# Kernel tuning notes

Hardware: AMD Instinct MI355X
Metric: run time of the kernel (lower is better)

## Reference

```python
import jax, jax.numpy as jnp
import numpy as np

EPS = 1e-8

def _center(G):
    # Double-centering: H @ G @ H with H = I - 11^T/n, expressed as mean subtraction.
    # Identical math to the torch H-matmul version, O(n^2) instead of O(n^3).
    row = jnp.mean(G, axis=-1, keepdims=True)
    col = jnp.mean(G, axis=-2, keepdims=True)
    tot = jnp.mean(G, axis=(-2, -1), keepdims=True)
    return G - row - col + tot


def setup_inputs() -> dict:
    key = jax.random.key(0)
    k1, k2 = jax.random.split(key)
    B, L, H, M = 32, 128, 512, 512
    x = jax.random.normal(k1, (B, L, H), dtype=jnp.float32)
    # nn.Embedding.from_pretrained(torch.normal(-0.01, 0.2, (M, L*H)))
    centroid_w = jax.random.normal(k2, (M, L * H), dtype=jnp.float32) * 0.2 - 0.01
    return {"x": x, "centroid_w": centroid_w}


def reference(x, centroid_w):
    B, L, H = x.shape
    M = centroid_w.shape[0]
    cent = centroid_w.reshape(M, L, H)

    # Centered linear Grams
    Cx = _center(jnp.einsum('blh,bkh->blk', x, x))        # (B, L, L)
    Cy = _center(jnp.einsum('mlh,mkh->mlk', cent, cent))  # (M, L, L)

    # linear HSIC: sum over LxL of elementwise product -> (B, M)
    hsic = jnp.einsum('bij,mij->bm', Cx, Cy)
    vx = jnp.sqrt(jnp.sum(Cx * Cx, axis=(1, 2)))  # (B,)  sqrt(HSIC(x,x))
    vy = jnp.sqrt(jnp.sum(Cy * Cy, axis=(1, 2)))  # (M,)  sqrt(HSIC(y,y))
    cka_loss_matrix = -jnp.log(jnp.abs(hsic / (vx[:, None] * vy[None, :])) + EPS)

    idx = jnp.argmax(cka_loss_matrix, axis=-1)  # (B,)
    sel = cent[idx]                              # (B, L, H) gathered centroids

    # Second CKA pass against selected centroids; torch broadcasting makes (B, B)
    Cs = _center(jnp.einsum('blh,bkh->blk', sel, sel))  # (B, L, L)
    hsic2 = jnp.einsum('bij,cij->bc', Cx, Cs)           # (B, B)
    vs = jnp.sqrt(jnp.sum(Cs * Cs, axis=(1, 2)))        # (B,)
    cka_loss = -jnp.log(jnp.mean(jnp.abs(hsic2 / (vx[:, None] * vs[None, :]))) + EPS)

    return cka_loss, cka_loss_matrix, idx
```

## Files before the change

kernel.cpp:

```cpp
#include <hip/hip_runtime.h>
#include <math.h>

#define BB 32
#define LL 128
#define HH 512
#define MM 512
#define NM 544
#define EPSF 1e-8f
#define CPLEN 10240
#define NCH 40

typedef __attribute__((ext_vector_type(8))) short short8b;
typedef __attribute__((ext_vector_type(4))) float f32x4;
typedef __attribute__((ext_vector_type(16))) float f32x16;

#define NWS_CP    0
#define NWS_PART  5570560
#define NWS_NSQ   6225920
#define NWS_HSIC  6226464
#define NWS_IDS   6242848

__device__ __forceinline__ unsigned pack2(unsigned lo, unsigned hi) {
    return (lo >> 16) | (hi & 0xffff0000u);
}

__device__ __forceinline__ void split3(const float4 lo, const float4 hi,
                                       uint4& p0, uint4& p1, uint4& p2) {
    float c[8] = {lo.x, lo.y, lo.z, lo.w, hi.x, hi.y, hi.z, hi.w};
    unsigned h[8], m[8], l[8];
#pragma unroll
    for (int i = 0; i < 8; ++i) {
        h[i] = __float_as_uint(c[i]) & 0xffff0000u;
        const float r1 = c[i] - __uint_as_float(h[i]);
        m[i] = __float_as_uint(r1) & 0xffff0000u;
        l[i] = __float_as_uint(r1 - __uint_as_float(m[i]));
    }
    p0 = make_uint4(pack2(h[0],h[1]), pack2(h[2],h[3]), pack2(h[4],h[5]), pack2(h[6],h[7]));
    p1 = make_uint4(pack2(m[0],m[1]), pack2(m[2],m[3]), pack2(m[4],m[5]), pack2(m[6],m[7]));
    p2 = make_uint4(pack2(l[0],l[1]), pack2(l[2],l[3]), pack2(l[4],l[5]), pack2(l[6],l[7]));
}

__device__ __forceinline__ void mfma6(f32x16& d, const short8b a[3], const short8b b[3]) {
    d = __builtin_amdgcn_mfma_f32_32x32x16_bf16(a[0], b[0], d, 0, 0, 0);
    d = __builtin_amdgcn_mfma_f32_32x32x16_bf16(a[0], b[1], d, 0, 0, 0);
    d = __builtin_amdgcn_mfma_f32_32x32x16_bf16(a[1], b[0], d, 0, 0, 0);
    d = __builtin_amdgcn_mfma_f32_32x32x16_bf16(a[1], b[1], d, 0, 0, 0);
    d = __builtin_amdgcn_mfma_f32_32x32x16_bf16(a[0], b[2], d, 0, 0, 0);
    d = __builtin_amdgcn_mfma_f32_32x32x16_bf16(a[2], b[0], d, 0, 0, 0);
}

__device__ __forceinline__ void ldstrip(const uint4* P, int strip, int lane, short8b f[3]) {
    const int s = lane >> 5;
    const int r = strip * 32 + (lane & 31);
#pragma unroll
    for (int p = 0; p < 3; ++p) {
        uint4 u = P[(p * 2 + s) * 128 + r];
        f[p] = *(const short8b*)&u;
    }
}

__device__ __forceinline__ int flatAB(int a, int b) {
    return ((a >> 3) * 2 + ((a >> 2) & 1)) * 128 + b * 4 + (a & 3);
}
__device__ __forceinline__ int Tix(int i, int j) {
    return i * (7 - i) / 2 + j;
}

__device__ __forceinline__ void put_tile(float* buf, int slot, const f32x16& a,
                                         int lane, bool add) {
    const int hi = lane >> 5, col = lane & 31;
#pragma unroll
    for (int c = 0; c < 4; ++c) {
        const int idx = slot * 1024 + (c * 2 + hi) * 128 + col * 4;
        f32x4 v;
        v[0] = a[c * 4 + 0]; v[1] = a[c * 4 + 1];
        v[2] = a[c * 4 + 2]; v[3] = a[c * 4 + 3];
        if (add) {
            const f32x4 o = *(const f32x4*)&buf[idx];
            v[0] += o[0]; v[1] += o[1]; v[2] += o[2]; v[3] += o[3];
        }
        *(f32x4*)&buf[idx] = v;
    }
}

__global__ __launch_bounds__(512, 4)
void gram8(const float* __restrict__ x,
           const float* __restrict__ cent,
           float* __restrict__ Cp,
           float* __restrict__ normsq)
{
    __shared__ __align__(16) unsigned char smraw[49152];
    __shared__ float rmv[128];
    __shared__ float red[512];
    __shared__ float gmsh;

    uint4* stage = (uint4*)smraw;
    float* buf   = (float*)smraw;

    const int tid  = threadIdx.x;
    const int lane = tid & 63;
    const int wid  = tid >> 6;
    const int g    = wid >> 2;
    const int gw   = wid & 3;
    const int n    = blockIdx.x;
    const float* Amat = (n < BB) ? (x + (size_t)n * LL * HH)
                                 : (cent + (size_t)(n - BB) * LL * HH);

    const int trow  = (tid >> 1) & 127;
    const int shalf = tid & 1;
    const float* rowp = Amat + (size_t)trow * HH + g * 256 + shalf * 8;

    f32x16 a0, a1, a2;
#pragma unroll
    for (int q = 0; q < 16; ++q) { a0[q] = 0.f; a1[q] = 0.f; a2[q] = 0.f; }

    float4 vA0 = *(const float4*)(rowp);
    float4 vA1 = *(const float4*)(rowp + 4);
    float4 vB0 = *(const float4*)(rowp + 16);
    float4 vB1 = *(const float4*)(rowp + 20);

#pragma unroll 2
    for (int t = 0; t < 16; ++t) {
        const int pb = t & 1;
        uint4 p0, p1, p2;
        if (pb == 0) split3(vA0, vA1, p0, p1, p2);
        else         split3(vB0, vB1, p0, p1, p2);

        uint4* SW = stage + g * 1536 + pb * 768;
        SW[(0 * 2 + shalf) * 128 + trow] = p0;
        SW[(1 * 2 + shalf) * 128 + trow] = p1;
        SW[(2 * 2 + shalf) * 128 + trow] = p2;

        if (t < 14) {
            const float* np = rowp + (t + 2) * 16;
            if (pb == 0) { vA0 = *(const float4*)np; vA1 = *(const float4*)(np + 4); }
            else         { vB0 = *(const float4*)np; vB1 = *(const float4*)(np + 4); }
        }

        __syncthreads();

        const uint4* Pr = stage + g * 1536 + pb * 768;
        short8b fa[3], fb[3];
        if (gw == 0) {
            ldstrip(Pr, 3, lane, fb);
            ldstrip(Pr, 0, lane, fa); mfma6(a0, fa, fb);
            ldstrip(Pr, 1, lane, fa); mfma6(a1, fa, fb);
            ldstrip(Pr, 2, lane, fa); mfma6(a2, fa, fb);
        } else if (gw == 1) {
            ldstrip(Pr, 3, lane, fa); mfma6(a0, fa, fa);
            ldstrip(Pr, 2, lane, fb);
            ldstrip(Pr, 0, lane, fa); mfma6(a1, fa, fb);
            ldstrip(Pr, 1, lane, fa); mfma6(a2, fa, fb);
        } else if (gw == 2) {
            ldstrip(Pr, 2, lane, fa); mfma6(a0, fa, fa);
            ldstrip(Pr, 0, lane, fa);
            ldstrip(Pr, 1, lane, fb); mfma6(a1, fa, fb);
        } else {
            ldstrip(Pr, 0, lane, fa); mfma6(a0, fa, fa);
            ldstrip(Pr, 1, lane, fa); mfma6(a1, fa, fa);
        }
    }

    __syncthreads();

    if (g == 0) {
        if (gw == 0)      { put_tile(buf, 3, a0, lane, false); put_tile(buf, 6, a1, lane, false); put_tile(buf, 8, a2, lane, false); }
        else if (gw == 1) { put_tile(buf, 9, a0, lane, false); put_tile(buf, 2, a1, lane, false); put_tile(buf, 5, a2, lane, false); }
        else if (gw == 2) { put_tile(buf, 7, a0, lane, false); put_tile(buf, 1, a1, lane, false); }
        else              { put_tile(buf, 0, a0, lane, false); put_tile(buf, 4, a1, lane, false); }
    }
    __syncthreads();
    if (g == 1) {
        if (gw == 0)      { put_tile(buf, 3, a0, lane, true); put_tile(buf, 6, a1, lane, true); put_tile(buf, 8, a2, lane, true); }
        else if (gw == 1) { put_tile(buf, 9, a0, lane, true); put_tile(buf, 2, a1, lane, true); put_tile(buf, 5, a2, lane, true); }
        else if (gw == 2) { put_tile(buf, 7, a0, lane, true); put_tile(buf, 1, a1, lane, true); }
        else              { put_tile(buf, 0, a0, lane, true); put_tile(buf, 4, a1, lane, true); }
    }
    __syncthreads();

    float Sv = 0.f;
    if (tid < 128) {
        const int i = tid >> 5, ri = tid & 31;
#pragma unroll
        for (int j = 0; j < 4; ++j) {
            if (j >= i) {
                const int gt = Tix(i, j);
#pragma unroll
                for (int b = 0; b < 32; ++b)
                    Sv += buf[gt * 1024 + flatAB(ri, b)];
            } else {
                const int gt = Tix(j, i);
#pragma unroll
                for (int a = 0; a < 32; ++a)
                    Sv += buf[gt * 1024 + flatAB(a, ri)];
            }
        }
        rmv[tid] = Sv * (1.f / 128.f);
    }
    red[tid] = (tid < 128) ? Sv : 0.f;
    __syncthreads();
    for (int s2 = 256; s2 > 0; s2 >>= 1) {
        if (tid < s2) red[tid] += red[tid + s2];
        __syncthreads();
    }
    if (tid == 0) gmsh = red[0] * (1.f / 16384.f);
    __syncthreads();
    const float gm = gmsh;

    float nsq = 0.f;
    float* dstn = Cp + (size_t)n * CPLEN;
#pragma unroll
    for (int u5 = 0; u5 < 5; ++u5) {
        const int u  = u5 * 512 + tid;
        const int gt = u >> 8;
        const int fo = (u & 255) * 4;
        const int c2 = fo >> 7;
        const int col = (fo >> 2) & 31;
        const int ar = (c2 >> 1) * 8 + (c2 & 1) * 4;
        int i, j;
        if (gt < 4)      { i = 0; j = gt; }
        else if (gt < 7) { i = 1; j = gt - 3; }
        else if (gt < 9) { i = 2; j = gt - 5; }
        else             { i = 3; j = 3; }
        const float sc = (i == j) ? 1.f : 1.41421356237309505f;
        const f32x4 vv = *(const f32x4*)&buf[u * 4];
        const float cj = rmv[j * 32 + col];
        f32x4 o;
#pragma unroll
        for (int q = 0; q < 4; ++q) {
            const float val = (vv[q] + gm - rmv[i * 32 + ar + q] - cj) * sc;
            nsq = fmaf(val, val, nsq);
            o[q] = val;
        }
        *(f32x4*)(dstn + u * 4) = o;
    }
    __syncthreads();
    red[tid] = nsq;
    __syncthreads();
    for (int s2 = 256; s2 > 0; s2 >>= 1) {
        if (tid < s2) red[tid] += red[tid + s2];
        __syncthreads();
    }
    if (tid == 0) normsq[n] = red[0];
}

__global__ __launch_bounds__(256, 2)
void hsic_partial(const float* __restrict__ Cp, float* __restrict__ part)
{
    __shared__ float cx[32][260];
    __shared__ float red2[256][16];

    const int tid = threadIdx.x;
    const int bx  = blockIdx.x;
    const int mt  = bx / NCH;
    const int kc  = bx % NCH;
    const int k0  = kc * 256;

#pragma unroll
    for (int i = 0; i < 8; ++i) {
        const int idx = i * 1024 + tid * 4;
        const int b = idx >> 8, k = idx & 255;
        *(float4*)&cx[b][k] = *(const float4*)&Cp[(size_t)b * CPLEN + k0 + k];
    }
    __syncthreads();

    const int kq = tid >> 6;
    const int bg = (tid >> 3) & 7;
    const int mg = tid & 7;
    const float* cyBase = Cp + (size_t)(BB + mt * 32 + mg * 4) * CPLEN + k0 + kq * 64;

    float a[4][4];
#pragma unroll
    for (int bi = 0; bi < 4; ++bi)
#pragma unroll
        for (int mi = 0; mi < 4; ++mi) a[bi][mi] = 0.f;

    for (int kk = 0; kk < 16; ++kk) {
        float4 cy[4];
#pragma unroll
        for (int mi = 0; mi < 4; ++mi)
            cy[mi] = *(const float4*)(cyBase + (size_t)mi * CPLEN + kk * 4);
        float4 cxv[4];
#pragma unroll
        for (int bi = 0; bi < 4; ++bi)
            cxv[bi] = *(const float4*)&cx[bg + bi * 8][kq * 64 + kk * 4];
#pragma unroll
        for (int bi = 0; bi < 4; ++bi)
#pragma unroll
            for (int mi = 0; mi < 4; ++mi) {
                a[bi][mi] = fmaf(cxv[bi].x, cy[mi].x, a[bi][mi]);
                a[bi][mi] = fmaf(cxv[bi].y, cy[mi].y, a[bi][mi]);
                a[bi][mi] = fmaf(cxv[bi].z, cy[mi].z, a[bi][mi]);
                a[bi][mi] = fmaf(cxv[bi].w, cy[mi].w, a[bi][mi]);
            }
    }

#pragma unroll
    for (int e = 0; e < 16; ++e) red2[tid][e] = a[e >> 2][e & 3];
    __syncthreads();
    if (tid < 64) {
#pragma unroll
        for (int e = 0; e < 16; ++e) {
            const float s = red2[tid][e] + red2[tid + 64][e] +
                            red2[tid + 128][e] + red2[tid + 192][e];
            const int bi = e >> 2, mi = e & 3;
            const int b = ((tid >> 3) & 7) + bi * 8;
            const int m = mt * 32 + (tid & 7) * 4 + mi;
            part[((size_t)kc * 32 + b) * 512 + m] = s;
        }
    }
}

__global__ __launch_bounds__(256)
void combine_loss(const float* __restrict__ part,
                  const float* __restrict__ normsq,
                  float* __restrict__ hsic,
                  int* __restrict__ ids,
                  float* __restrict__ out)
{
    __shared__ float rv[256];
    __shared__ int   ri[256];
    const int b = blockIdx.x;
    const int tid = threadIdx.x;
    const float vx = sqrtf(normsq[b]);

    float best = -INFINITY; int bm = 0;
    for (int m = tid; m < MM; m += 256) {
        float s = 0.f;
        for (int kc = 0; kc < NCH; ++kc)
            s += part[((size_t)kc * 32 + b) * 512 + m];
        hsic[b * MM + m] = s;
        const float vy = sqrtf(normsq[BB + m]);
        const float loss = -logf(fabsf(s) / (vx * vy) + EPSF);
        out[1 + b * MM + m] = loss;
        if (loss > best) { best = loss; bm = m; }
    }
    rv[tid] = best; ri[tid] = bm;
    __syncthreads();
    for (int s2 = 128; s2 > 0; s2 >>= 1) {
        if (tid < s2) {
            if (rv[tid + s2] > rv[tid] ||
                (rv[tid + s2] == rv[tid] && ri[tid + s2] < ri[tid])) {
                rv[tid] = rv[tid + s2]; ri[tid] = ri[tid + s2];
            }
        }
        __syncthreads();
    }
    if (tid == 0) { ids[b] = ri[0]; out[1 + BB * MM + b] = (float)ri[0]; }
}

__global__ __launch_bounds__(1024)
void scalar_loss(const float* __restrict__ hsic,
                 const float* __restrict__ normsq,
                 const int* __restrict__ ids,
                 float* __restrict__ out)
{
    __shared__ float red[1024];
    const int tid = threadIdx.x;
    const int b = tid >> 5, c = tid & 31;
    const int m = ids[c];
    red[tid] = fabsf(hsic[b * MM + m]) /
               (sqrtf(normsq[b]) * sqrtf(normsq[BB + m]));
    __syncthreads();
    for (int s = 512; s > 0; s >>= 1) {
        if (tid < s) red[tid] += red[tid + s];
        __syncthreads();
    }
    if (tid == 0) out[0] = -logf(red[0] * (1.f / 1024.f) + EPSF);
}

extern "C" void kernel_launch(void* const* d_in, const int* in_sizes, int n_in,
                              void* d_out, int out_size, void* d_ws, size_t ws_size,
                              hipStream_t stream) {
    const float* x    = (const float*)d_in[0];
    const float* cent = (const float*)d_in[1];
    float* out = (float*)d_out;
    float* ws  = (float*)d_ws;

    float* Cp     = ws + NWS_CP;
    float* part   = ws + NWS_PART;
    float* normsq = ws + NWS_NSQ;
    float* hsic   = ws + NWS_HSIC;
    int*   ids    = (int*)(ws + NWS_IDS);

    gram8<<<NM, 512, 0, stream>>>(x, cent, Cp, normsq);
    hsic_partial<<<16 * NCH, 256, 0, stream>>>(Cp, part);
    combine_loss<<<BB, 256, 0, stream>>>(part, normsq, hsic, ids, out);
    scalar_loss<<<1, 1024, 0, stream>>>(hsic, normsq, ids, out);
}
```

Measured before the change: 96.39 us.

## Replace gram kernel with barrier-free per-wave async LDS loading pipeline

The Gram kernel now has each wave stream its own 32-row strips from global memory straight into a private swizzled LDS slice using global_load_lds, double-buffered with vmcnt waits. This removes the block-wide __syncthreads in the main K loop, and each wave does its own bf16x3 split after reading from LDS. Waves are assigned tile pairs so that only the strips they need are loaded. The cost is 80KB of LDS, launch bounds of one block per CU (lower occupancy), and redundant loads and splits of shared strips across waves.

```diff
diff --git a/kernel.cpp b/kernel.cpp
--- a/kernel.cpp
+++ b/kernel.cpp
@@ -9,6 +9,7 @@
 #define EPSF 1e-8f
 #define CPLEN 10240
 #define NCH 40
+#define R2C 1.41421356237309505f
 
 typedef __attribute__((ext_vector_type(8))) short short8b;
 typedef __attribute__((ext_vector_type(4))) float f32x4;
@@ -19,6 +20,9 @@
 #define NWS_NSQ   6225920
 #define NWS_HSIC  6226464
 #define NWS_IDS   6242848
+
+#define AS1(p) ((const __attribute__((address_space(1))) void*)(p))
+#define AS3(p) ((__attribute__((address_space(3))) void*)(p))
 
 __device__ __forceinline__ unsigned pack2(unsigned lo, unsigned hi) {
     return (lo >> 16) | (hi & 0xffff0000u);
@@ -47,16 +51,6 @@
     d = __builtin_amdgcn_mfma_f32_32x32x16_bf16(a[1], b[1], d, 0, 0, 0);
     d = __builtin_amdgcn_mfma_f32_32x32x16_bf16(a[0], b[2], d, 0, 0, 0);
     d = __builtin_amdgcn_mfma_f32_32x32x16_bf16(a[2], b[0], d, 0, 0, 0);
-}
-
-__device__ __forceinline__ void ldstrip(const uint4* P, int strip, int lane, short8b f[3]) {
-    const int s = lane >> 5;
-    const int r = strip * 32 + (lane & 31);
-#pragma unroll
-    for (int p = 0; p < 3; ++p) {
-        uint4 u = P[(p * 2 + s) * 128 + r];
-        f[p] = *(const short8b*)&u;
-    }
 }
 
 __device__ __forceinline__ int flatAB(int a, int b) {
@@ -83,98 +77,123 @@
     }
 }
 
-__global__ __launch_bounds__(512, 4)
-void gram8(const float* __restrict__ x,
-           const float* __restrict__ cent,
-           float* __restrict__ Cp,
-           float* __restrict__ normsq)
+template<int NS, int S0, int S1, int S2>
+__device__ __forceinline__ void wave_main(const float* __restrict__ Amat,
+                                          char* slice, int khalf, int lane,
+                                          f32x16& t0, f32x16& t1, f32x16& t2)
 {
-    __shared__ __align__(16) unsigned char smraw[49152];
+    const int gsrc  = (lane & 3) ^ ((lane >> 3) & 3);
+    const int rowin = lane >> 2;
+    const int SS[3] = {S0, S1, S2};
+
+    const float* srcb[NS][2];
+#pragma unroll
+    for (int s = 0; s < NS; ++s)
+#pragma unroll
+        for (int ih = 0; ih < 2; ++ih)
+            srcb[s][ih] = Amat + (size_t)(SS[s] * 32 + ih * 16 + rowin) * HH
+                          + khalf * 256 + gsrc * 4;
+
+#pragma unroll
+    for (int s = 0; s < NS; ++s)
+#pragma unroll
+        for (int ih = 0; ih < 2; ++ih)
+            __builtin_amdgcn_global_load_lds(AS1(srcb[s][ih]),
+                AS3(slice + s * 4096 + ih * 1024), 16, 0, 0);
+
+    const int r31 = lane & 31;
+    const int oct = lane >> 5;
+    const int sw  = (r31 >> 1) & 3;
+    const int off0 = ((2 * oct) ^ sw) << 4;
+    const int off1 = ((2 * oct + 1) ^ sw) << 4;
+
+#pragma unroll 2
+    for (int t = 0; t < 16; ++t) {
+        const int pb = t & 1;
+        if (t < 15) {
+#pragma unroll
+            for (int s = 0; s < NS; ++s)
+#pragma unroll
+                for (int ih = 0; ih < 2; ++ih)
+                    __builtin_amdgcn_global_load_lds(
+                        AS1(srcb[s][ih] + (t + 1) * 16),
+                        AS3(slice + s * 4096 + (pb ^ 1) * 2048 + ih * 1024),
+                        16, 0, 0);
+            if constexpr (NS == 2)
+                asm volatile("s_waitcnt vmcnt(4)" ::: "memory");
+            else
+                asm volatile("s_waitcnt vmcnt(6)" ::: "memory");
+        } else {
+            asm volatile("s_waitcnt vmcnt(0)" ::: "memory");
+        }
+        short8b fr[3][3];
+#pragma unroll
+        for (int s = 0; s < NS; ++s) {
+            const char* rp = slice + s * 4096 + pb * 2048 + r31 * 64;
+            const float4 lo = *(const float4*)(rp + off0);
+            const float4 hi = *(const float4*)(rp + off1);
+            uint4 q0, q1, q2;
+            split3(lo, hi, q0, q1, q2);
+            fr[s][0] = *(short8b*)&q0;
+            fr[s][1] = *(short8b*)&q1;
+            fr[s][2] = *(short8b*)&q2;
+        }
+        if constexpr (NS == 2) {
+            mfma6(t0, fr[0], fr[0]);
+            mfma6(t1, fr[0], fr[1]);
+            mfma6(t2, fr[1], fr[1]);
+        } else {
+            mfma6(t0, fr[0], fr[1]);
+            mfma6(t1, fr[0], fr[2]);
+        }
+    }
+}
+
+__global__ __launch_bounds__(512, 1)
+void gram_free(const float* __restrict__ x,
+               const float* __restrict__ cent,
+               float* __restrict__ Cp,
+               float* __restrict__ normsq)
+{
+    __shared__ __align__(16) char smem[81920];
     __shared__ float rmv[128];
     __shared__ float red[512];
     __shared__ float gmsh;
 
-    uint4* stage = (uint4*)smraw;
-    float* buf   = (float*)smraw;
-
-    const int tid  = threadIdx.x;
-    const int lane = tid & 63;
-    const int wid  = tid >> 6;
-    const int g    = wid >> 2;
-    const int gw   = wid & 3;
-    const int n    = blockIdx.x;
+    const int tid = threadIdx.x, lane = tid & 63, wid = tid >> 6;
+    const int n = blockIdx.x;
     const float* Amat = (n < BB) ? (x + (size_t)n * LL * HH)
                                  : (cent + (size_t)(n - BB) * LL * HH);
 
-    const int trow  = (tid >> 1) & 127;
-    const int shalf = tid & 1;
-    const float* rowp = Amat + (size_t)trow * HH + g * 256 + shalf * 8;
-
-    f32x16 a0, a1, a2;
-#pragma unroll
-    for (int q = 0; q < 16; ++q) { a0[q] = 0.f; a1[q] = 0.f; a2[q] = 0.f; }
-
-    float4 vA0 = *(const float4*)(rowp);
-    float4 vA1 = *(const float4*)(rowp + 4);
-    float4 vB0 = *(const float4*)(rowp + 16);
-    float4 vB1 = *(const float4*)(rowp + 20);
-
-#pragma unroll 2
-    for (int t = 0; t < 16; ++t) {
-        const int pb = t & 1;
-        uint4 p0, p1, p2;
-        if (pb == 0) split3(vA0, vA1, p0, p1, p2);
-        else         split3(vB0, vB1, p0, p1, p2);
-
-        uint4* SW = stage + g * 1536 + pb * 768;
-        SW[(0 * 2 + shalf) * 128 + trow] = p0;
-        SW[(1 * 2 + shalf) * 128 + trow] = p1;
-        SW[(2 * 2 + shalf) * 128 + trow] = p2;
-
-        if (t < 14) {
-            const float* np = rowp + (t + 2) * 16;
-            if (pb == 0) { vA0 = *(const float4*)np; vA1 = *(const float4*)(np + 4); }
-            else         { vB0 = *(const float4*)np; vB1 = *(const float4*)(np + 4); }
-        }
-
-        __syncthreads();
-
-        const uint4* Pr = stage + g * 1536 + pb * 768;
-        short8b fa[3], fb[3];
-        if (gw == 0) {
-            ldstrip(Pr, 3, lane, fb);
-            ldstrip(Pr, 0, lane, fa); mfma6(a0, fa, fb);
-            ldstrip(Pr, 1, lane, fa); mfma6(a1, fa, fb);
-            ldstrip(Pr, 2, lane, fa); mfma6(a2, fa, fb);
-        } else if (gw == 1) {
-            ldstrip(Pr, 3, lane, fa); mfma6(a0, fa, fa);
-            ldstrip(Pr, 2, lane, fb);
-            ldstrip(Pr, 0, lane, fa); mfma6(a1, fa, fb);
-            ldstrip(Pr, 1, lane, fa); mfma6(a2, fa, fb);
-        } else if (gw == 2) {
-            ldstrip(Pr, 2, lane, fa); mfma6(a0, fa, fa);
-            ldstrip(Pr, 0, lane, fa);
-            ldstrip(Pr, 1, lane, fb); mfma6(a1, fa, fb);
-        } else {
-            ldstrip(Pr, 0, lane, fa); mfma6(a0, fa, fa);
-            ldstrip(Pr, 1, lane, fa); mfma6(a1, fa, fa);
-        }
-    }
-
-    __syncthreads();
-
-    if (g == 0) {
-        if (gw == 0)      { put_tile(buf, 3, a0, lane, false); put_tile(buf, 6, a1, lane, false); put_tile(buf, 8, a2, lane, false); }
-        else if (gw == 1) { put_tile(buf, 9, a0, lane, false); put_tile(buf, 2, a1, lane, false); put_tile(buf, 5, a2, lane, false); }
-        else if (gw == 2) { put_tile(buf, 7, a0, lane, false); put_tile(buf, 1, a1, lane, false); }
-        else              { put_tile(buf, 0, a0, lane, false); put_tile(buf, 4, a1, lane, false); }
-    }
-    __syncthreads();
-    if (g == 1) {
-        if (gw == 0)      { put_tile(buf, 3, a0, lane, true); put_tile(buf, 6, a1, lane, true); put_tile(buf, 8, a2, lane, true); }
-        else if (gw == 1) { put_tile(buf, 9, a0, lane, true); put_tile(buf, 2, a1, lane, true); put_tile(buf, 5, a2, lane, true); }
-        else if (gw == 2) { put_tile(buf, 7, a0, lane, true); put_tile(buf, 1, a1, lane, true); }
-        else              { put_tile(buf, 0, a0, lane, true); put_tile(buf, 4, a1, lane, true); }
+    const int khalf = wid >> 2;
+    const int g     = wid & 3;
+    char* slice = smem + khalf * 40960 + g * 8192 + (g == 3 ? 4096 : 0);
+
+    f32x16 t0, t1, t2;
+#pragma unroll
+    for (int q = 0; q < 16; ++q) { t0[q] = 0.f; t1[q] = 0.f; t2[q] = 0.f; }
+
+    switch (g) {
+        case 0:  wave_main<2, 0, 1, 0>(Amat, slice, khalf, lane, t0, t1, t2); break;
+        case 1:  wave_main<2, 2, 3, 0>(Amat, slice, khalf, lane, t0, t1, t2); break;
+        case 2:  wave_main<3, 0, 2, 3>(Amat, slice, khalf, lane, t0, t1, t2); break;
+        default: wave_main<3, 1, 2, 3>(Amat, slice, khalf, lane, t0, t1, t2); break;
+    }
+
+    __syncthreads();
+    float* buf = (float*)smem;
+    if (wid < 4) {
+        if (g == 0)      { put_tile(buf, 0, t0, lane, false); put_tile(buf, 1, t1, lane, false); put_tile(buf, 4, t2, lane, false); }
+        else if (g == 1) { put_tile(buf, 7, t0, lane, false); put_tile(buf, 8, t1, lane, false); put_tile(buf, 9, t2, lane, false); }
+        else if (g == 2) { put_tile(buf, 2, t0, lane, false); put_tile(buf, 3, t1, lane, false); }
+        else             { put_tile(buf, 5, t0, lane, false); put_tile(buf, 6, t1, lane, false); }
+    }
+    __syncthreads();
+    if (wid >= 4) {
+        if (g == 0)      { put_tile(buf, 0, t0, lane, true); put_tile(buf, 1, t1, lane, true); put_tile(buf, 4, t2, lane, true); }
+        else if (g == 1) { put_tile(buf, 7, t0, lane, true); put_tile(buf, 8, t1, lane, true); put_tile(buf, 9, t2, lane, true); }
+        else if (g == 2) { put_tile(buf, 2, t0, lane, true); put_tile(buf, 3, t1, lane, true); }
+        else             { put_tile(buf, 5, t0, lane, true); put_tile(buf, 6, t1, lane, true); }
     }
     __syncthreads();
 
@@ -222,7 +241,7 @@
         else if (gt < 7) { i = 1; j = gt - 3; }
         else if (gt < 9) { i = 2; j = gt - 5; }
         else             { i = 3; j = 3; }
-        const float sc = (i == j) ? 1.f : 1.41421356237309505f;
+        const float sc = (i == j) ? 1.f : R2C;
         const f32x4 vv = *(const f32x4*)&buf[u * 4];
         const float cj = rmv[j * 32 + col];
         f32x4 o;
@@ -383,7 +402,7 @@
     float* hsic   = ws + NWS_HSIC;
     int*   ids    = (int*)(ws + NWS_IDS);
 
-    gram8<<<NM, 512, 0, stream>>>(x, cent, Cp, normsq);
+    gram_free<<<NM, 512, 0, stream>>>(x, cent, Cp, normsq);
     hsic_partial<<<16 * NCH, 256, 0, stream>>>(Cp, part);
     combine_loss<<<BB, 256, 0, stream>>>(part, normsq, hsic, ids, out);
     scalar_loss<<<1, 1024, 0, stream>>>(hsic, normsq, ids, out);
```

Result: slower. 103.8 us (+7.7%).
